# Performance work log

Measured on AMD Instinct MI355X. Metric: run time of the kernel, lower is better.

Reference implementation:

```python
import jax, jax.numpy as jnp
import numpy as np

NUM_HEADS = 8
EPS = 1e-5


def conv3x3(x, w):
    # x: (b,c,f,w), w: (out_c,in_c,3,3), padding=1, stride=1, no bias
    return jax.lax.conv_general_dilated(
        x, w, window_strides=(1, 1), padding=((1, 1), (1, 1)),
        dimension_numbers=('NCHW', 'OIHW', 'NCHW'))


def mc_layernorm(x, g, b):
    # MultichannelLayerNorm: layernorm over the feature axis (dim 2),
    # per-(channel, feature) affine.
    m = jnp.mean(x, axis=2, keepdims=True)
    v = jnp.var(x, axis=2, keepdims=True)
    xn = (x - m) * jax.lax.rsqrt(v + EPS)
    return xn * g[None, :, :, None] + b[None, :, :, None]


def mc_linear(x, wp, wd=None):
    # per-channel feature linear: y[b,c,g,w] = sum_f wp[c,g,f] x[b,c,f,w]
    y = jnp.einsum('bcfw,cgf->bcgw', x, wp)
    if wd is not None:  # depthwise=True adds 1x1 cross-channel mix
        y = jnp.einsum('bcfw,oc->bofw', y, wd)
    return y


def _split_heads(t):
    # (b,c,f,w) -> (b,c,w,H,dh); matches transpose(2,3).reshape(b,c,w,H,-1)
    b, c, f, w = t.shape
    return jnp.transpose(t, (0, 1, 3, 2)).reshape(b, c, w, NUM_HEADS, f // NUM_HEADS)


def _forward(x, conv_q, conv_k, conv_v, wq, wk, wv, wo_pw, wo_dw,
             g1, b1, g2, b2, w1_pw, w1_dw, w2_pw):
    b, c, f, w = x.shape
    # --- attention (MultichannelMultiheadAttention, prev_qk=None) ---
    n1 = mc_layernorm(x, g1, b1)
    q = _split_heads(mc_linear(conv3x3(n1, conv_q), wq))  # (b,c,w,H,dh)
    k = _split_heads(mc_linear(conv3x3(n1, conv_k), wk))
    v = _split_heads(mc_linear(conv3x3(n1, conv_v), wv))
    # qk: (b,c,H,w,w); scaled by sqrt(features) (torch uses sqrt(h)=height)
    qk = jnp.einsum('bcqhd,bckhd->bchqk', q, k) / jnp.sqrt(jnp.float32(f))
    a = jnp.einsum('bchqk,bckhd->bcqhd', jax.nn.softmax(qk, axis=-1), v)
    a = jnp.transpose(a.reshape(b, c, w, f), (0, 1, 3, 2))  # (b,c,f,w)
    z = mc_linear(a, wo_pw, wo_dw)  # o_proj, depthwise=True
    h = x + z  # dropout is identity in eval
    # --- FFN with SquaredReLU ---
    n2 = mc_layernorm(h, g2, b2)
    u = mc_linear(n2, w1_pw, w1_dw)          # (b,c,4f,w)
    u = jnp.square(jax.nn.relu(u))           # SquaredReLU
    z = mc_linear(u, w2_pw)                  # (b,c,f,w)
    h = h + z
    return h, qk


def setup_inputs() -> dict:
    key = jax.random.key(0)
    ks = jax.random.split(key, 12)
    b, c, f, w = 2, 16, 256, 512
    e = 4 * f
    s_conv = 1.0 / np.sqrt(c * 9)
    s_f = 1.0 / np.sqrt(f)
    s_e = 1.0 / np.sqrt(e)
    s_c = 1.0 / np.sqrt(c)
    return {
        'x': jax.random.normal(ks[0], (b, c, f, w), jnp.float32),
        'conv_q': jax.random.normal(ks[1], (c, c, 3, 3), jnp.float32) * s_conv,
        'conv_k': jax.random.normal(ks[2], (c, c, 3, 3), jnp.float32) * s_conv,
        'conv_v': jax.random.normal(ks[3], (c, c, 3, 3), jnp.float32) * s_conv,
        'wq': jax.random.normal(ks[4], (c, f, f), jnp.float32) * s_f,
        'wk': jax.random.normal(ks[5], (c, f, f), jnp.float32) * s_f,
        'wv': jax.random.normal(ks[6], (c, f, f), jnp.float32) * s_f,
        'wo_pw': jax.random.normal(ks[7], (c, f, f), jnp.float32) * s_f,
        'wo_dw': jax.random.normal(ks[8], (c, c), jnp.float32) * s_c,
        'g1': jnp.ones((c, f), jnp.float32),
        'b1': jnp.zeros((c, f), jnp.float32),
        'g2': jnp.ones((c, f), jnp.float32),
        'b2': jnp.zeros((c, f), jnp.float32),
        'w1_pw': jax.random.normal(ks[9], (c, e, f), jnp.float32) * s_f,
        'w1_dw': jax.random.normal(ks[10], (c, c), jnp.float32) * s_c,
        'w2_pw': jax.random.normal(ks[11], (c, f, e), jnp.float32) * s_e,
    }


def reference(x, conv_q, conv_k, conv_v, wq, wk, wv, wo_pw, wo_dw,
              g1, b1, g2, b2, w1_pw, w1_dw, w2_pw):
    return _forward(x, conv_q, conv_k, conv_v, wq, wk, wv, wo_pw, wo_dw,
                    g1, b1, g2, b2, w1_pw, w1_dw, w2_pw)
```

## Files before the change

kernel.cpp:

```cpp
#include <hip/hip_runtime.h>

#define BB 2
#define CC 16
#define BC 32
#define FF 256
#define WW 512
#define HH 8
#define DH 32

using bf16x8 = __attribute__((ext_vector_type(8))) __bf16;
using f32x4  = __attribute__((ext_vector_type(4))) float;
using us8    = __attribute__((ext_vector_type(8))) unsigned short;
using us4    = __attribute__((ext_vector_type(4))) unsigned short;

#define AS1 __attribute__((address_space(1)))
#define AS3 __attribute__((address_space(3)))

__device__ __forceinline__ float bf2f(unsigned short u) {
    union { unsigned int i; float f; } x; x.i = ((unsigned int)u) << 16; return x.f;
}
__device__ __forceinline__ unsigned short f2bf(float f) {
    union { float f; unsigned int i; } x; x.f = f;
    unsigned int r = x.i + 0x7fffu + ((x.i >> 16) & 1u);
    return (unsigned short)(r >> 16);
}
__device__ __forceinline__ f32x4 mfma16(bf16x8 a, bf16x8 b, f32x4 c) {
    return __builtin_amdgcn_mfma_f32_16x16x32_bf16(a, b, c, 0, 0, 0);
}
__device__ __forceinline__ void gload16(const void* g, void* l) {
    __builtin_amdgcn_global_load_lds((AS1 void*)g, (AS3 void*)l, 16, 0, 0);
}

__global__ __launch_bounds__(256) void prep_ln(
    const float* __restrict__ x, const float* __restrict__ g1,
    const float* __restrict__ b1, unsigned short* __restrict__ n1,
    const float* __restrict__ wq, const float* __restrict__ wk,
    const float* __restrict__ wv, const float* __restrict__ wo,
    const float* __restrict__ w1, const float* __restrict__ w2,
    const float* __restrict__ cwq, const float* __restrict__ cwk,
    const float* __restrict__ cwv,
    unsigned short* __restrict__ Wqkv, unsigned short* __restrict__ Wo16,
    unsigned short* __restrict__ W116, unsigned short* __restrict__ W216,
    unsigned short* __restrict__ Aw) {
    __shared__ float red[2][4][64];
    __shared__ float mr[2][64];
    int bid = blockIdx.x;
    if (bid < 256) {
        int bc = bid & 31, c = bc & 15;
        int part = threadIdx.x >> 6, wl = threadIdx.x & 63;
        int w = (bid >> 5) * 64 + wl;
        const float* xp = x + ((size_t)bc * FF + part * 64) * WW + w;
        float s = 0.f, s2 = 0.f;
#pragma unroll 4
        for (int i = 0; i < 64; ++i) { float t = xp[(size_t)i * WW]; s += t; s2 += t * t; }
        red[0][part][wl] = s; red[1][part][wl] = s2;
        __syncthreads();
        if (part == 0) {
            float S  = red[0][0][wl] + red[0][1][wl] + red[0][2][wl] + red[0][3][wl];
            float S2 = red[1][0][wl] + red[1][1][wl] + red[1][2][wl] + red[1][3][wl];
            float m = S * (1.f / FF);
            float v = S2 * (1.f / FF) - m * m;
            mr[0][wl] = m; mr[1][wl] = rsqrtf(v + 1e-5f);
        }
        __syncthreads();
        float m = mr[0][wl], r = mr[1][wl];
        const float* gp = g1 + c * FF + part * 64;
        const float* bp = b1 + c * FF + part * 64;
        unsigned short* op = n1 + ((size_t)bc * FF + part * 64) * WW + w;
#pragma unroll 4
        for (int i = 0; i < 64; ++i)
            op[(size_t)i * WW] = f2bf((xp[(size_t)i * WW] - m) * r * gp[i] + bp[i]);
    } else if (bid < 256 + 6144) {
        int i = (bid - 256) * 256 + threadIdx.x;
        const float* s; unsigned short* d; int off;
        if (i < 131072)       { s = wq; d = Wqkv;            off = i; }
        else if (i < 262144)  { s = wk; d = Wqkv + 1048576;  off = i - 131072; }
        else if (i < 393216)  { s = wv; d = Wqkv + 2097152;  off = i - 262144; }
        else if (i < 524288)  { s = wo; d = Wo16;            off = i - 393216; }
        else if (i < 1048576) { s = w1; d = W116;            off = i - 524288; }
        else                  { s = w2; d = W216;            off = i - 1048576; }
        const float4* sp = (const float4*)s + (size_t)off * 2;
        float4 a = sp[0], b = sp[1];
        us8 p;
        p[0] = f2bf(a.x); p[1] = f2bf(a.y); p[2] = f2bf(a.z); p[3] = f2bf(a.w);
        p[4] = f2bf(b.x); p[5] = f2bf(b.y); p[6] = f2bf(b.z); p[7] = f2bf(b.w);
        *((us8*)d + off) = p;
    } else {
        int idx = (bid - 256 - 6144) * 256 + threadIdx.x;
        if (idx < 7680) {
            int tensor = idx / 2560;
            int r = idx - tensor * 2560;
            int tp = r >> 9, co = (r >> 5) & 15, k = r & 31;
            int tap = tp * 2 + (k >> 4), ci = k & 15;
            float v = 0.f;
            if (tap < 9) {
                const float* w = tensor == 0 ? cwq : (tensor == 1 ? cwk : cwv);
                v = w[(co * 16 + ci) * 9 + tap];
            }
            Aw[idx] = f2bf(v);
        }
    }
}

__global__ __launch_bounds__(256) void ln2t_kernel(
    const float* __restrict__ x, const float* __restrict__ g,
    const float* __restrict__ bta, unsigned short* __restrict__ out) {
    __shared__ float red[2][4][64];
    __shared__ float mr[2][64];
    int bc = blockIdx.x, c = bc & 15;
    int part = threadIdx.x >> 6, wl = threadIdx.x & 63;
    int w = blockIdx.y * 64 + wl;
    const float* xp = x + ((size_t)bc * FF + part * 64) * WW + w;
    float s = 0.f, s2 = 0.f;
#pragma unroll 4
    for (int i = 0; i < 64; ++i) { float t = xp[(size_t)i * WW]; s += t; s2 += t * t; }
    red[0][part][wl] = s; red[1][part][wl] = s2;
    __syncthreads();
    if (part == 0) {
        float S  = red[0][0][wl] + red[0][1][wl] + red[0][2][wl] + red[0][3][wl];
        float S2 = red[1][0][wl] + red[1][1][wl] + red[1][2][wl] + red[1][3][wl];
        float m = S * (1.f / FF);
        float v = S2 * (1.f / FF) - m * m;
        mr[0][wl] = m; mr[1][wl] = rsqrtf(v + 1e-5f);
    }
    __syncthreads();
    float m = mr[0][wl], r = mr[1][wl];
    const float* gp = g + c * FF + part * 64;
    const float* bp = bta + c * FF + part * 64;
    unsigned short* op = out + ((size_t)bc * WW + w) * FF + part * 64;
    for (int i8 = 0; i8 < 8; ++i8) {
        us8 pk;
#pragma unroll
        for (int e = 0; e < 8; ++e) {
            int i = i8 * 8 + e;
            pk[e] = f2bf((xp[(size_t)i * WW] - m) * r * gp[i] + bp[i]);
        }
        *(us8*)(op + i8 * 8) = pk;
    }
}

__global__ __launch_bounds__(256) void conv3_mfma(
    const unsigned short* __restrict__ n1, const unsigned short* __restrict__ Aw,
    unsigned short* __restrict__ oq, unsigned short* __restrict__ ok,
    unsigned short* __restrict__ ov) {
    __shared__ __align__(16) unsigned short Xl[6][68][16];
    const int b = blockIdx.z;
    const int f0 = blockIdx.y * 4;
    const int w0 = blockIdx.x * 64;
    const int tx = threadIdx.x;
    const int lane = tx & 63, wid = tx >> 6;
    const int lr = lane & 15, lg = lane >> 4;
    {
        uint4 z{0, 0, 0, 0};
        for (int i = tx; i < 816; i += 256) ((uint4*)Xl)[i] = z;
    }
    __syncthreads();
    if (tx < 240) {
        int c = tx % 10;
        int fr = (tx / 10) % 6;
        int ci0 = (tx / 60) * 4;
        int fy = f0 - 1 + fr;
        int wx = w0 - 8 + c * 8;
        if (fy >= 0 && fy < FF && wx >= 0 && wx <= WW - 8) {
            const unsigned short* base = n1 + ((size_t)(b * CC + ci0) * FF + fy) * WW + wx;
            us8 v0 = *(const us8*)(base);
            us8 v1 = *(const us8*)(base + (size_t)FF * WW);
            us8 v2 = *(const us8*)(base + (size_t)2 * FF * WW);
            us8 v3 = *(const us8*)(base + (size_t)3 * FF * WW);
            if (c >= 1 && c <= 8) {
#pragma unroll
                for (int e = 0; e < 8; ++e) {
                    int wl = c * 8 + e - 7;
                    us4 p; p.x = v0[e]; p.y = v1[e]; p.z = v2[e]; p.w = v3[e];
                    *(us4*)(&Xl[fr][wl][ci0]) = p;
                }
            } else {
#pragma unroll
                for (int e = 0; e < 8; ++e) {
                    int wl = c * 8 + e - 7;
                    if (wl >= 0 && wl < 66) {
                        us4 p; p.x = v0[e]; p.y = v1[e]; p.z = v2[e]; p.w = v3[e];
                        *(us4*)(&Xl[fr][wl][ci0]) = p;
                    }
                }
            }
        }
    }
    __syncthreads();
    bf16x8 A[3][5];
#pragma unroll
    for (int t3 = 0; t3 < 3; ++t3)
#pragma unroll
        for (int t = 0; t < 5; ++t)
            A[t3][t] = *(const bf16x8*)(Aw + ((t3 * 5 + t) * 16 + lr) * 32 + lg * 8);
    const bool h = (lane & 32) != 0;
    int doff[5];
    doff[0] = (h ? (-68 * 32) : ((-68 - 1) * 32));
    doff[1] = (h ? (-1 * 32) : ((-68 + 1) * 32));
    doff[2] = (h ? (1 * 32) : 0);
    doff[3] = (h ? (68 * 32) : ((68 - 1) * 32));
    doff[4] = ((68 + 1) * 32);
    const int fl = wid + 1;
    const int fglob = f0 + wid;
    char* xbase = (char*)Xl + (fl * 68 + 1) * 32 + ((lg & 1) ? 16 : 0);
#pragma unroll
    for (int pt = 0; pt < 4; ++pt) {
        char* bb = xbase + (pt * 16 + lr) * 32;
        bf16x8 Bf[5];
#pragma unroll
        for (int t = 0; t < 5; ++t) Bf[t] = *(const bf16x8*)(bb + doff[t]);
        f32x4 aq = {0.f, 0.f, 0.f, 0.f}, ak = {0.f, 0.f, 0.f, 0.f}, av = {0.f, 0.f, 0.f, 0.f};
#pragma unroll
        for (int t = 0; t < 5; ++t) {
            aq = mfma16(A[0][t], Bf[t], aq);
            ak = mfma16(A[1][t], Bf[t], ak);
            av = mfma16(A[2][t], Bf[t], av);
        }
        int w = w0 + pt * 16 + lr;
#pragma unroll
        for (int r = 0; r < 4; ++r) {
            int co = lg * 4 + r;
            size_t o = ((size_t)(b * CC + co) * FF + fglob) * WW + w;
            oq[o] = f2bf(aq[r]);
            ok[o] = f2bf(ak[r]);
            ov[o] = f2bf(av[r]);
        }
    }
}

template <int K, int BSRC, int MODE, int NT>
__global__ __launch_bounds__(256, 4) void mgemm3(
    const unsigned short* __restrict__ Wb, const unsigned short* __restrict__ T,
    unsigned short* __restrict__ ob, float* __restrict__ of) {
    constexpr int M = 256;
    __shared__ __align__(16) unsigned short Al[64 * 64];
    __shared__ __align__(16) unsigned short Bl[128 * 64];
    const int id = blockIdx.x;
    const int grp = ((id >> 5) << 3) | (id & 7);
    const int g = (id >> 3) & 3;
    const int t = (NT > 1) ? (grp >> 7) : 0;
    const int rem = grp & 127;
    const int bc = rem >> 2, z = rem & 3;
    const int c = bc & 15;
    const int G0 = g * 64, W0 = z * 128;
    const int tx = threadIdx.x;
    const int lane = tx & 63, wid = tx >> 6;
    const int lr = lane & 15, lg = lane >> 4;
    const int wr = wid >> 1, wc = wid & 1;
    const unsigned short* Ab = Wb + (size_t)t * 1048576 + ((size_t)c * M + G0) * K;
    const unsigned short* Tt = T + (size_t)t * 4194304;
    f32x4 acc[2][4];
#pragma unroll
    for (int i = 0; i < 2; ++i)
#pragma unroll
        for (int j = 0; j < 4; ++j) acc[i][j] = (f32x4){0.f, 0.f, 0.f, 0.f};

    const int arow0 = tx >> 3;

    for (int f0 = 0; f0 < K; f0 += 64) {
#pragma unroll
        for (int rep = 0; rep < 2; ++rep) {
            int row = arow0 + rep * 32;
            int seg = (tx & 7) ^ (row & 7);
            gload16(Ab + (size_t)row * K + f0 + seg * 8,
                    (char*)Al + wid * 1024 + rep * 4096);
        }
        if (BSRC == 0) {
            const unsigned short* Tb = Tt + ((size_t)bc * WW + W0) * K;
#pragma unroll
            for (int rep = 0; rep < 4; ++rep) {
                int row = arow0 + rep * 32;
                int seg = (tx & 7) ^ (row & 7) ^ ((row >> 3) & 7);
                gload16(Tb + (size_t)row * K + f0 + seg * 8,
                        (char*)Bl + wid * 1024 + rep * 4096);
            }
        } else {
            const unsigned short* Tb = Tt + (size_t)bc * K * WW;
            const int wseg = tx & 15, fgrp = tx >> 4;
            us8 tv[4];
#pragma unroll
            for (int i = 0; i < 4; ++i)
                tv[i] = *(const us8*)(Tb + (size_t)(f0 + fgrp * 4 + i) * WW + W0 + wseg * 8);
#pragma unroll
            for (int j = 0; j < 8; ++j) {
                int w = wseg * 8 + j;
                us4 p; p.x = tv[0][j]; p.y = tv[1][j]; p.z = tv[2][j]; p.w = tv[3][j];
                *(us4*)((char*)Bl + w * 128 +
                        ((((fgrp >> 1) ^ (w & 7) ^ ((w >> 3) & 7)) << 4)) + (fgrp & 1) * 8) = p;
            }
        }
        __syncthreads();
#pragma unroll
        for (int kc = 0; kc < 2; ++kc) {
            bf16x8 af[2], bf[4];
#pragma unroll
            for (int i = 0; i < 2; ++i) {
                int gr = wr * 32 + i * 16 + lr;
                af[i] = *(const bf16x8*)((char*)Al + gr * 128 +
                        (((kc * 4 + lg) ^ (gr & 7)) << 4));
            }
#pragma unroll
            for (int j = 0; j < 4; ++j) {
                int wrw = wc * 64 + j * 16 + lr;
                bf[j] = *(const bf16x8*)((char*)Bl + wrw * 128 +
                        (((kc * 4 + lg) ^ (wrw & 7) ^ ((wrw >> 3) & 7)) << 4));
            }
#pragma unroll
            for (int i = 0; i < 2; ++i)
#pragma unroll
                for (int j = 0; j < 4; ++j)
                    acc[i][j] = mfma16(af[i], bf[j], acc[i][j]);
        }
        __syncthreads();
    }
#pragma unroll
    for (int i = 0; i < 2; ++i)
#pragma unroll
        for (int j = 0; j < 4; ++j) {
            int g2 = G0 + wr * 32 + i * 16 + lg * 4;
            int w = W0 + wc * 64 + j * 16 + lr;
#pragma unroll
            for (int r = 0; r < 4; ++r) {
                size_t o = (size_t)t * 4194304 + ((size_t)bc * M + g2 + r) * WW + w;
                if (MODE == 0) ob[o] = f2bf(acc[i][j][r]);
                else of[o] += acc[i][j][r];
            }
        }
}

template <int K, int M, int MODE>
__global__ __launch_bounds__(256, 2) void mgemm2(
    const unsigned short* __restrict__ Wb, const unsigned short* __restrict__ T,
    unsigned short* __restrict__ ob, float* __restrict__ of) {
    __shared__ __align__(16) unsigned short SH[2][128 * 64];
    unsigned short* Al = SH[0];
    unsigned short* Bl = SH[1];
    const int id = blockIdx.x;
    const int grp = ((id >> 6) << 3) | (id & 7);
    const int g = (id >> 3) & 7;
    const int bc = grp >> 2, z = grp & 3;
    const int c = bc & 15;
    const int G0 = g * 128, W0 = z * 128;
    const int tx = threadIdx.x;
    const int lane = tx & 63, wid = tx >> 6;
    const int lr = lane & 15, lg = lane >> 4;
    const int wr = wid >> 1, wc = wid & 1;
    const unsigned short* Ab = Wb + ((size_t)c * M + G0) * K;
    f32x4 acc[4][4];
#pragma unroll
    for (int i = 0; i < 4; ++i)
#pragma unroll
        for (int j = 0; j < 4; ++j) acc[i][j] = (f32x4){0.f, 0.f, 0.f, 0.f};

    const int arow0 = tx >> 3;

    for (int f0 = 0; f0 < K; f0 += 64) {
#pragma unroll
        for (int rep = 0; rep < 4; ++rep) {
            int row = arow0 + rep * 32;
            int seg = (tx & 7) ^ (row & 7);
            gload16(Ab + (size_t)row * K + f0 + seg * 8,
                    (char*)Al + wid * 1024 + rep * 4096);
        }
        {
            const unsigned short* Tb = T + ((size_t)bc * WW + W0) * K;
#pragma unroll
            for (int rep = 0; rep < 4; ++rep) {
                int row = arow0 + rep * 32;
                int seg = (tx & 7) ^ (row & 7) ^ ((row >> 3) & 7);
                gload16(Tb + (size_t)row * K + f0 + seg * 8,
                        (char*)Bl + wid * 1024 + rep * 4096);
            }
        }
        __syncthreads();
#pragma unroll
        for (int kc = 0; kc < 2; ++kc) {
            bf16x8 af[4], bf[4];
#pragma unroll
            for (int i = 0; i < 4; ++i) {
                int gr = wr * 64 + i * 16 + lr;
                af[i] = *(const bf16x8*)((char*)Al + gr * 128 +
                        (((kc * 4 + lg) ^ (gr & 7)) << 4));
                int wrw = wc * 64 + i * 16 + lr;
                bf[i] = *(const bf16x8*)((char*)Bl + wrw * 128 +
                        (((kc * 4 + lg) ^ (wrw & 7) ^ ((wrw >> 3) & 7)) << 4));
            }
#pragma unroll
            for (int i = 0; i < 4; ++i)
#pragma unroll
                for (int j = 0; j < 4; ++j)
                    acc[i][j] = mfma16(af[i], bf[j], acc[i][j]);
        }
        __syncthreads();
    }
    if (MODE == 2) {
        char* S = (char*)SH;
#pragma unroll
        for (int i = 0; i < 4; ++i)
#pragma unroll
            for (int j = 0; j < 4; ++j) {
                int wl = wc * 64 + j * 16 + lr;
                int gl = wr * 64 + i * 16 + lg * 4;
                us4 pk;
                pk.x = f2bf(acc[i][j][0]); pk.y = f2bf(acc[i][j][1]);
                pk.z = f2bf(acc[i][j][2]); pk.w = f2bf(acc[i][j][3]);
                *(us4*)(S + wl * 256 + ((gl * 2) ^ ((wl & 7) << 4))) = pk;
            }
        __syncthreads();
        unsigned short* og = ob + ((size_t)bc * WW + W0) * M + G0;
#pragma unroll
        for (int rep = 0; rep < 8; ++rep) {
            int slot = tx + rep * 256;
            int row = slot >> 4, col = slot & 15;
            us8 v = *(const us8*)(S + row * 256 + ((col * 16) ^ ((row & 7) << 4)));
            *(us8*)(og + (size_t)row * M + col * 8) = v;
        }
    } else {
#pragma unroll
        for (int i = 0; i < 4; ++i)
#pragma unroll
            for (int j = 0; j < 4; ++j) {
                int gg = G0 + wr * 64 + i * 16 + lg * 4;
                int w = W0 + wc * 64 + j * 16 + lr;
#pragma unroll
                for (int r = 0; r < 4; ++r) {
                    size_t o = ((size_t)bc * M + gg + r) * WW + w;
                    if (MODE == 0) ob[o] = f2bf(acc[i][j][r]);
                    else of[o] += acc[i][j][r];
                }
            }
    }
}

__global__ __launch_bounds__(256, 2) void attn_fused(
    const unsigned short* __restrict__ qb, const unsigned short* __restrict__ kb,
    const unsigned short* __restrict__ vb, float* __restrict__ qko,
    unsigned short* __restrict__ abT) {
    __shared__ unsigned short Kl[512 * 32];
    __shared__ unsigned short Vl[32 * 512];
    __shared__ unsigned short Ql[64 * 32];
    const int bch = blockIdx.x, qt = blockIdx.y;
    const int bc = bch >> 3, h = bch & 7;
    const int tx = threadIdx.x;
    const int lane = tx & 63, wid = tx >> 6;
    const int lr = lane & 15, lg = lane >> 4;

    const unsigned short* kbase = kb + ((size_t)bc * FF + h * DH) * WW;
    const unsigned short* vbase = vb + ((size_t)bc * FF + h * DH) * WW;
    const unsigned short* qbase = qb + ((size_t)bc * FF + h * DH) * WW + qt * 64;

    {
        int d0 = ((tx >> 3) & 7) * 4;
#pragma unroll
        for (int rep = 0; rep < 2; ++rep) {
            int kw0 = (tx & 7) * 8 + ((tx >> 6) & 3) * 64 + rep * 256;
            us8 v0 = *(const us8*)(kbase + (size_t)(d0 + 0) * WW + kw0);
            us8 v1 = *(const us8*)(kbase + (size_t)(d0 + 1) * WW + kw0);
            us8 v2 = *(const us8*)(kbase + (size_t)(d0 + 2) * WW + kw0);
            us8 v3 = *(const us8*)(kbase + (size_t)(d0 + 3) * WW + kw0);
#pragma unroll
            for (int j = 0; j < 8; ++j) {
                int kw = kw0 + j;
                us4 p; p.x = v0[j]; p.y = v1[j]; p.z = v2[j]; p.w = v3[j];
                *(us4*)((char*)Kl + kw * 64 + ((d0 * 2) ^ ((kw & 3) << 4))) = p;
            }
        }
    }
    {
        int d = tx >> 3;
        int sw = (d & 7) << 4;
#pragma unroll
        for (int rep = 0; rep < 8; ++rep) {
            int kw0 = (tx & 7) * 8 + rep * 64;
            us8 tv = *(const us8*)(vbase + (size_t)d * WW + kw0);
            *(us8*)((char*)Vl + d * 1024 + ((kw0 * 2) ^ sw)) = tv;
        }
    }
    if (tx < 64) {
        int d0 = ((tx >> 3) & 7) * 4;
        int q0 = (tx & 7) * 8;
        us8 v0 = *(const us8*)(qbase + (size_t)(d0 + 0) * WW + q0);
        us8 v1 = *(const us8*)(qbase + (size_t)(d0 + 1) * WW + q0);
        us8 v2 = *(const us8*)(qbase + (size_t)(d0 + 2) * WW + q0);
        us8 v3 = *(const us8*)(qbase + (size_t)(d0 + 3) * WW + q0);
#pragma unroll
        for (int j = 0; j < 8; ++j) {
            us4 p; p.x = v0[j]; p.y = v1[j]; p.z = v2[j]; p.w = v3[j];
            *(us4*)(&Ql[(q0 + j) * 32 + d0]) = p;
        }
    }
    __syncthreads();

    const int q0w = wid * 16;
    bf16x8 qf = *(const bf16x8*)((char*)Ql + (q0w + lr) * 64 + lg * 16);
    f32x4 s[32];
#pragma unroll
    for (int i = 0; i < 32; ++i) s[i] = (f32x4){0.f, 0.f, 0.f, 0.f};
#pragma unroll
    for (int kwt = 0; kwt < 32; ++kwt) {
        int krow = kwt * 16 + lr;
        bf16x8 kf = *(const bf16x8*)((char*)Kl + krow * 64 + ((lg * 16) ^ ((krow & 3) << 4)));
        s[kwt] = mfma16(kf, qf, s[kwt]);
    }
    float mx = -3.0e38f;
    float* qrow = qko + ((size_t)bch * WW + qt * 64 + q0w + lr) * WW;
#pragma unroll
    for (int kwt = 0; kwt < 32; ++kwt) {
        s[kwt] *= 0.0625f;
        float4 st;
        st.x = s[kwt][0]; st.y = s[kwt][1]; st.z = s[kwt][2]; st.w = s[kwt][3];
        *(float4*)(qrow + kwt * 16 + lg * 4) = st;
        mx = fmaxf(mx, fmaxf(fmaxf(st.x, st.y), fmaxf(st.z, st.w)));
    }
    mx = fmaxf(mx, __shfl_xor(mx, 16));
    mx = fmaxf(mx, __shfl_xor(mx, 32));
    float sum = 0.f;
#pragma unroll
    for (int kwt = 0; kwt < 32; ++kwt) {
#pragma unroll
        for (int r = 0; r < 4; ++r) {
            float p = __expf(s[kwt][r] - mx);
            s[kwt][r] = p;
            sum += p;
        }
    }
    sum += __shfl_xor(sum, 16);
    sum += __shfl_xor(sum, 32);
    float inv = 1.0f / sum;

    f32x4 av[2];
    av[0] = (f32x4){0.f, 0.f, 0.f, 0.f};
    av[1] = (f32x4){0.f, 0.f, 0.f, 0.f};
#pragma unroll
    for (int t = 0; t < 16; ++t) {
        unsigned pa0 = f2bf(s[2 * t][0]) | ((unsigned)f2bf(s[2 * t][1]) << 16);
        unsigned pa1 = f2bf(s[2 * t][2]) | ((unsigned)f2bf(s[2 * t][3]) << 16);
        unsigned pb0 = f2bf(s[2 * t + 1][0]) | ((unsigned)f2bf(s[2 * t + 1][1]) << 16);
        unsigned pb1 = f2bf(s[2 * t + 1][2]) | ((unsigned)f2bf(s[2 * t + 1][3]) << 16);
        unsigned s16_0 = (lg == 1) ? pa0 : pb0, s16_1 = (lg == 1) ? pa1 : pb1;
        unsigned s32_0 = (lg == 3) ? pa0 : pb0, s32_1 = (lg == 3) ? pa1 : pb1;
        unsigned s48_0 = (lg == 2) ? pa0 : pb0, s48_1 = (lg == 2) ? pa1 : pb1;
        unsigned r16_0 = (unsigned)__shfl_xor((int)s16_0, 16);
        unsigned r16_1 = (unsigned)__shfl_xor((int)s16_1, 16);
        unsigned r32_0 = (unsigned)__shfl_xor((int)s32_0, 32);
        unsigned r32_1 = (unsigned)__shfl_xor((int)s32_1, 32);
        unsigned r48_0 = (unsigned)__shfl_xor((int)s48_0, 48);
        unsigned r48_1 = (unsigned)__shfl_xor((int)s48_1, 48);
        uint4 wv;
        if (lg == 0)      { wv.x = pa0;   wv.y = pa1;   wv.z = r16_0; wv.w = r16_1; }
        else if (lg == 1) { wv.x = r48_0; wv.y = r48_1; wv.z = r32_0; wv.w = r32_1; }
        else if (lg == 2) { wv.x = r32_0; wv.y = r32_1; wv.z = r48_0; wv.w = r48_1; }
        else              { wv.x = r16_0; wv.y = r16_1; wv.z = pb0;  wv.w = pb1; }
        bf16x8 pf = *reinterpret_cast<bf16x8*>(&wv);
#pragma unroll
        for (int di = 0; di < 2; ++di) {
            int vr = di * 16 + lr;
            bf16x8 vf = *(const bf16x8*)((char*)Vl + vr * 1024 + ((t * 64 + lg * 16) ^ ((vr & 7) << 4)));
            av[di] = mfma16(vf, pf, av[di]);
        }
    }
    unsigned short* arow = abT + ((size_t)bc * WW + qt * 64 + q0w + lr) * FF + h * DH;
#pragma unroll
    for (int di = 0; di < 2; ++di) {
        us4 pk;
        pk.x = f2bf(av[di][0] * inv); pk.y = f2bf(av[di][1] * inv);
        pk.z = f2bf(av[di][2] * inv); pk.w = f2bf(av[di][3] * inv);
        *(us4*)(arow + di * 16 + lg * 4) = pk;
    }
}

template <int NPC, int MODE>
__global__ __launch_bounds__(256) void dwmix(
    const unsigned short* __restrict__ in, const float* __restrict__ wdw,
    const float* __restrict__ x, float* __restrict__ fo, unsigned short* __restrict__ bo) {
    __shared__ unsigned short L[16][1024];
    int b = blockIdx.y;
    size_t base = (size_t)blockIdx.x * 1024;
    int tx = threadIdx.x;
#pragma unroll
    for (int r = 0; r < 8; ++r) {
        int idx = tx + r * 256;
        int ci = idx >> 7;
        int seg = idx & 127;
        *(us8*)&L[ci][seg * 8] = *(const us8*)(in + ((size_t)(b * 16 + ci)) * NPC + base + seg * 8);
    }
    __syncthreads();
#pragma unroll
    for (int pos = 0; pos < 4; ++pos) {
        int fw = tx + pos * 256;
        float vin[16];
#pragma unroll
        for (int ci = 0; ci < 16; ++ci) vin[ci] = bf2f(L[ci][fw]);
#pragma unroll
        for (int o = 0; o < 16; ++o) {
            float s = 0.f;
#pragma unroll
            for (int ci = 0; ci < 16; ++ci) s += wdw[o * 16 + ci] * vin[ci];
            size_t oi = ((size_t)(b * 16 + o)) * NPC + base + fw;
            if (MODE == 0) fo[oi] = x[oi] + s;
            else { s = fmaxf(s, 0.f); bo[oi] = f2bf(s * s); }
        }
    }
}

extern "C" void kernel_launch(void* const* d_in, const int* in_sizes, int n_in,
                              void* d_out, int out_size, void* d_ws, size_t ws_size,
                              hipStream_t stream) {
    const float* x      = (const float*)d_in[0];
    const float* conv_q = (const float*)d_in[1];
    const float* conv_k = (const float*)d_in[2];
    const float* conv_v = (const float*)d_in[3];
    const float* wq     = (const float*)d_in[4];
    const float* wk     = (const float*)d_in[5];
    const float* wv     = (const float*)d_in[6];
    const float* wo_pw  = (const float*)d_in[7];
    const float* wo_dw  = (const float*)d_in[8];
    const float* g1     = (const float*)d_in[9];
    const float* b1     = (const float*)d_in[10];
    const float* g2     = (const float*)d_in[11];
    const float* b2     = (const float*)d_in[12];
    const float* w1_pw  = (const float*)d_in[13];
    const float* w1_dw  = (const float*)d_in[14];
    const float* w2_pw  = (const float*)d_in[15];

    float* hout  = (float*)d_out;
    float* qkout = (float*)d_out + 4194304;

    char* ws = (char*)d_ws;
    const size_t MB1 = (size_t)1 << 20;
    unsigned short* n1   = (unsigned short*)(ws + 0 * MB1);
    unsigned short* cq   = (unsigned short*)(ws + 8 * MB1);
    unsigned short* qb   = (unsigned short*)(ws + 32 * MB1);
    unsigned short* kb   = (unsigned short*)(ws + 40 * MB1);
    unsigned short* vb   = (unsigned short*)(ws + 48 * MB1);
    unsigned short* abT  = (unsigned short*)(ws + 56 * MB1);
    unsigned short* pwb  = (unsigned short*)(ws + 64 * MB1);
    unsigned short* n2t  = (unsigned short*)(ws + 72 * MB1);
    unsigned short* u1t  = (unsigned short*)(ws + 80 * MB1);
    unsigned short* u2t  = (unsigned short*)(ws + 112 * MB1);
    unsigned short* Wqkv = (unsigned short*)(ws + 144 * MB1);
    unsigned short* Wo16 = (unsigned short*)(ws + 150 * MB1);
    unsigned short* W116 = (unsigned short*)(ws + 152 * MB1);
    unsigned short* W216 = (unsigned short*)(ws + 160 * MB1);
    unsigned short* Awb  = (unsigned short*)(ws + 168 * MB1);

    prep_ln<<<dim3(6430), 256, 0, stream>>>(x, g1, b1, n1,
                                            wq, wk, wv, wo_pw, w1_pw, w2_pw,
                                            conv_q, conv_k, conv_v,
                                            Wqkv, Wo16, W116, W216, Awb);
    conv3_mfma<<<dim3(8, 64, BB), 256, 0, stream>>>(n1, Awb, cq, cq + 4194304, cq + 8388608);
    mgemm3<256, 1, 0, 3><<<dim3(1536), 256, 0, stream>>>(Wqkv, cq, qb, nullptr);
    attn_fused<<<dim3(BC * HH, 8), 256, 0, stream>>>(qb, kb, vb, qkout, abT);
    mgemm3<256, 0, 0, 1><<<dim3(512), 256, 0, stream>>>(Wo16, abT, pwb, nullptr);
    dwmix<131072, 0><<<dim3(128, BB), 256, 0, stream>>>(pwb, wo_dw, x, hout, nullptr);
    ln2t_kernel<<<dim3(BC, 8), 256, 0, stream>>>(hout, g2, b2, n2t);
    mgemm2<256, 1024, 2><<<dim3(1024), 256, 0, stream>>>(W116, n2t, u1t, nullptr);
    dwmix<524288, 1><<<dim3(512, BB), 256, 0, stream>>>(u1t, w1_dw, nullptr, nullptr, u2t);
    mgemm3<1024, 0, 1, 1><<<dim3(512), 256, 0, stream>>>(W216, u2t, nullptr, hout);
}
```

Measured before the change: 269.2 us.

## Double-buffer mgemm3 K-loop, read V from global, and enlarge grids of small kernels

mgemm3 gets double-buffered LDS tiles so the next K-slice loads while the current one runs its MFMAs, and its occupancy hint drops from 4 to 3 blocks to make room for the larger LDS footprint. attn_fused stops staging V in LDS and reads V fragments directly from global memory, which frees LDS. The layernorm kernels now use 32-wide column tiles and dwmix gets a tile template, so the first dwmix launch uses 256-element tiles. Together these give more blocks for the bandwidth-bound kernels. The costs are more LDS per mgemm3 block, lower occupancy, and uncoalesced V reads in attention.

```diff
diff --git a/kernel.cpp b/kernel.cpp
--- a/kernel.cpp
+++ b/kernel.cpp
@@ -42,36 +42,37 @@
     unsigned short* __restrict__ Wqkv, unsigned short* __restrict__ Wo16,
     unsigned short* __restrict__ W116, unsigned short* __restrict__ W216,
     unsigned short* __restrict__ Aw) {
-    __shared__ float red[2][4][64];
-    __shared__ float mr[2][64];
+    __shared__ float red[2][8][32];
+    __shared__ float mr[2][32];
     int bid = blockIdx.x;
-    if (bid < 256) {
+    if (bid < 512) {
         int bc = bid & 31, c = bc & 15;
-        int part = threadIdx.x >> 6, wl = threadIdx.x & 63;
-        int w = (bid >> 5) * 64 + wl;
-        const float* xp = x + ((size_t)bc * FF + part * 64) * WW + w;
+        int part = threadIdx.x >> 5, wl = threadIdx.x & 31;
+        int w = (bid >> 5) * 32 + wl;
+        const float* xp = x + ((size_t)bc * FF + part * 32) * WW + w;
         float s = 0.f, s2 = 0.f;
 #pragma unroll 4
-        for (int i = 0; i < 64; ++i) { float t = xp[(size_t)i * WW]; s += t; s2 += t * t; }
+        for (int i = 0; i < 32; ++i) { float t = xp[(size_t)i * WW]; s += t; s2 += t * t; }
         red[0][part][wl] = s; red[1][part][wl] = s2;
         __syncthreads();
         if (part == 0) {
-            float S  = red[0][0][wl] + red[0][1][wl] + red[0][2][wl] + red[0][3][wl];
-            float S2 = red[1][0][wl] + red[1][1][wl] + red[1][2][wl] + red[1][3][wl];
+            float S = 0.f, S2 = 0.f;
+#pragma unroll
+            for (int p = 0; p < 8; ++p) { S += red[0][p][wl]; S2 += red[1][p][wl]; }
             float m = S * (1.f / FF);
             float v = S2 * (1.f / FF) - m * m;
             mr[0][wl] = m; mr[1][wl] = rsqrtf(v + 1e-5f);
         }
         __syncthreads();
         float m = mr[0][wl], r = mr[1][wl];
-        const float* gp = g1 + c * FF + part * 64;
-        const float* bp = b1 + c * FF + part * 64;
-        unsigned short* op = n1 + ((size_t)bc * FF + part * 64) * WW + w;
+        const float* gp = g1 + c * FF + part * 32;
+        const float* bp = b1 + c * FF + part * 32;
+        unsigned short* op = n1 + ((size_t)bc * FF + part * 32) * WW + w;
 #pragma unroll 4
-        for (int i = 0; i < 64; ++i)
+        for (int i = 0; i < 32; ++i)
             op[(size_t)i * WW] = f2bf((xp[(size_t)i * WW] - m) * r * gp[i] + bp[i]);
-    } else if (bid < 256 + 6144) {
-        int i = (bid - 256) * 256 + threadIdx.x;
+    } else if (bid < 512 + 6144) {
+        int i = (bid - 512) * 256 + threadIdx.x;
         const float* s; unsigned short* d; int off;
         if (i < 131072)       { s = wq; d = Wqkv;            off = i; }
         else if (i < 262144)  { s = wk; d = Wqkv + 1048576;  off = i - 131072; }
@@ -86,7 +87,7 @@
         p[4] = f2bf(b.x); p[5] = f2bf(b.y); p[6] = f2bf(b.z); p[7] = f2bf(b.w);
         *((us8*)d + off) = p;
     } else {
-        int idx = (bid - 256 - 6144) * 256 + threadIdx.x;
+        int idx = (bid - 512 - 6144) * 256 + threadIdx.x;
         if (idx < 7680) {
             int tensor = idx / 2560;
             int r = idx - tensor * 2560;
@@ -105,30 +106,31 @@
 __global__ __launch_bounds__(256) void ln2t_kernel(
     const float* __restrict__ x, const float* __restrict__ g,
     const float* __restrict__ bta, unsigned short* __restrict__ out) {
-    __shared__ float red[2][4][64];
-    __shared__ float mr[2][64];
+    __shared__ float red[2][8][32];
+    __shared__ float mr[2][32];
     int bc = blockIdx.x, c = bc & 15;
-    int part = threadIdx.x >> 6, wl = threadIdx.x & 63;
-    int w = blockIdx.y * 64 + wl;
-    const float* xp = x + ((size_t)bc * FF + part * 64) * WW + w;
+    int part = threadIdx.x >> 5, wl = threadIdx.x & 31;
+    int w = blockIdx.y * 32 + wl;
+    const float* xp = x + ((size_t)bc * FF + part * 32) * WW + w;
     float s = 0.f, s2 = 0.f;
 #pragma unroll 4
-    for (int i = 0; i < 64; ++i) { float t = xp[(size_t)i * WW]; s += t; s2 += t * t; }
+    for (int i = 0; i < 32; ++i) { float t = xp[(size_t)i * WW]; s += t; s2 += t * t; }
     red[0][part][wl] = s; red[1][part][wl] = s2;
     __syncthreads();
     if (part == 0) {
-        float S  = red[0][0][wl] + red[0][1][wl] + red[0][2][wl] + red[0][3][wl];
-        float S2 = red[1][0][wl] + red[1][1][wl] + red[1][2][wl] + red[1][3][wl];
+        float S = 0.f, S2 = 0.f;
+#pragma unroll
+        for (int p = 0; p < 8; ++p) { S += red[0][p][wl]; S2 += red[1][p][wl]; }
         float m = S * (1.f / FF);
         float v = S2 * (1.f / FF) - m * m;
         mr[0][wl] = m; mr[1][wl] = rsqrtf(v + 1e-5f);
     }
     __syncthreads();
     float m = mr[0][wl], r = mr[1][wl];
-    const float* gp = g + c * FF + part * 64;
-    const float* bp = bta + c * FF + part * 64;
-    unsigned short* op = out + ((size_t)bc * WW + w) * FF + part * 64;
-    for (int i8 = 0; i8 < 8; ++i8) {
+    const float* gp = g + c * FF + part * 32;
+    const float* bp = bta + c * FF + part * 32;
+    unsigned short* op = out + ((size_t)bc * WW + w) * FF + part * 32;
+    for (int i8 = 0; i8 < 4; ++i8) {
         us8 pk;
 #pragma unroll
         for (int e = 0; e < 8; ++e) {
@@ -229,12 +231,13 @@
 }
 
 template <int K, int BSRC, int MODE, int NT>
-__global__ __launch_bounds__(256, 4) void mgemm3(
+__global__ __launch_bounds__(256, 3) void mgemm3(
     const unsigned short* __restrict__ Wb, const unsigned short* __restrict__ T,
     unsigned short* __restrict__ ob, float* __restrict__ of) {
     constexpr int M = 256;
-    __shared__ __align__(16) unsigned short Al[64 * 64];
-    __shared__ __align__(16) unsigned short Bl[128 * 64];
+    constexpr int NK = K / 64;
+    __shared__ __align__(16) unsigned short Al[2][64 * 64];
+    __shared__ __align__(16) unsigned short Bl[2][128 * 64];
     const int id = blockIdx.x;
     const int grp = ((id >> 5) << 3) | (id & 7);
     const int g = (id >> 3) & 3;
@@ -249,60 +252,70 @@
     const int wr = wid >> 1, wc = wid & 1;
     const unsigned short* Ab = Wb + (size_t)t * 1048576 + ((size_t)c * M + G0) * K;
     const unsigned short* Tt = T + (size_t)t * 4194304;
+    const unsigned short* TbB0 = Tt + ((size_t)bc * WW + W0) * K;
+    const unsigned short* TbB1 = Tt + (size_t)bc * K * WW;
+    const int arow0 = tx >> 3;
+    const int wseg = tx & 15, fgrp = tx >> 4;
     f32x4 acc[2][4];
 #pragma unroll
     for (int i = 0; i < 2; ++i)
 #pragma unroll
         for (int j = 0; j < 4; ++j) acc[i][j] = (f32x4){0.f, 0.f, 0.f, 0.f};
 
-    const int arow0 = tx >> 3;
-
-    for (int f0 = 0; f0 < K; f0 += 64) {
-#pragma unroll
-        for (int rep = 0; rep < 2; ++rep) {
-            int row = arow0 + rep * 32;
-            int seg = (tx & 7) ^ (row & 7);
-            gload16(Ab + (size_t)row * K + f0 + seg * 8,
-                    (char*)Al + wid * 1024 + rep * 4096);
-        }
-        if (BSRC == 0) {
-            const unsigned short* Tb = Tt + ((size_t)bc * WW + W0) * K;
-#pragma unroll
-            for (int rep = 0; rep < 4; ++rep) {
-                int row = arow0 + rep * 32;
-                int seg = (tx & 7) ^ (row & 7) ^ ((row >> 3) & 7);
-                gload16(Tb + (size_t)row * K + f0 + seg * 8,
-                        (char*)Bl + wid * 1024 + rep * 4096);
-            }
-        } else {
-            const unsigned short* Tb = Tt + (size_t)bc * K * WW;
-            const int wseg = tx & 15, fgrp = tx >> 4;
-            us8 tv[4];
-#pragma unroll
-            for (int i = 0; i < 4; ++i)
-                tv[i] = *(const us8*)(Tb + (size_t)(f0 + fgrp * 4 + i) * WW + W0 + wseg * 8);
-#pragma unroll
-            for (int j = 0; j < 8; ++j) {
-                int w = wseg * 8 + j;
-                us4 p; p.x = tv[0][j]; p.y = tv[1][j]; p.z = tv[2][j]; p.w = tv[3][j];
-                *(us4*)((char*)Bl + w * 128 +
-                        ((((fgrp >> 1) ^ (w & 7) ^ ((w >> 3) & 7)) << 4)) + (fgrp & 1) * 8) = p;
-            }
-        }
-        __syncthreads();
+#define STAGE_A(buf, f0)                                                     \
+    _Pragma("unroll")                                                        \
+    for (int rep = 0; rep < 2; ++rep) {                                      \
+        int row = arow0 + rep * 32;                                          \
+        int seg = (tx & 7) ^ (row & 7);                                      \
+        gload16(Ab + (size_t)row * K + (f0) + seg * 8,                       \
+                (char*)Al[buf] + wid * 1024 + rep * 4096);                   \
+    }
+#define STAGE_B0(buf, f0)                                                    \
+    _Pragma("unroll")                                                        \
+    for (int rep = 0; rep < 4; ++rep) {                                      \
+        int row = arow0 + rep * 32;                                          \
+        int seg = (tx & 7) ^ (row & 7) ^ ((row >> 3) & 7);                   \
+        gload16(TbB0 + (size_t)row * K + (f0) + seg * 8,                     \
+                (char*)Bl[buf] + wid * 1024 + rep * 4096);                   \
+    }
+#define GATHER_B1(f0)                                                        \
+    _Pragma("unroll")                                                        \
+    for (int i = 0; i < 4; ++i)                                              \
+        tv[i] = *(const us8*)(TbB1 + (size_t)((f0) + fgrp * 4 + i) * WW + W0 + wseg * 8);
+#define WRITE_B1(buf)                                                        \
+    _Pragma("unroll")                                                        \
+    for (int j = 0; j < 8; ++j) {                                            \
+        int w = wseg * 8 + j;                                                \
+        us4 p; p.x = tv[0][j]; p.y = tv[1][j]; p.z = tv[2][j]; p.w = tv[3][j]; \
+        *(us4*)((char*)Bl[buf] + w * 128 +                                   \
+                ((((fgrp >> 1) ^ (w & 7) ^ ((w >> 3) & 7)) << 4)) + (fgrp & 1) * 8) = p; \
+    }
+
+    us8 tv[4];
+    STAGE_A(0, 0)
+    if (BSRC == 0) { STAGE_B0(0, 0) } else { GATHER_B1(0) WRITE_B1(0) }
+    __syncthreads();
+    int cur = 0;
+    for (int k = 0; k < NK; ++k) {
+        const int f0n = (k + 1) * 64;
+        if (k + 1 < NK) {
+            STAGE_A(cur ^ 1, f0n)
+            if (BSRC == 0) { STAGE_B0(cur ^ 1, f0n) }
+            else { GATHER_B1(f0n) }
+        }
 #pragma unroll
         for (int kc = 0; kc < 2; ++kc) {
             bf16x8 af[2], bf[4];
 #pragma unroll
             for (int i = 0; i < 2; ++i) {
                 int gr = wr * 32 + i * 16 + lr;
-                af[i] = *(const bf16x8*)((char*)Al + gr * 128 +
+                af[i] = *(const bf16x8*)((char*)Al[cur] + gr * 128 +
                         (((kc * 4 + lg) ^ (gr & 7)) << 4));
             }
 #pragma unroll
             for (int j = 0; j < 4; ++j) {
                 int wrw = wc * 64 + j * 16 + lr;
-                bf[j] = *(const bf16x8*)((char*)Bl + wrw * 128 +
+                bf[j] = *(const bf16x8*)((char*)Bl[cur] + wrw * 128 +
                         (((kc * 4 + lg) ^ (wrw & 7) ^ ((wrw >> 3) & 7)) << 4));
             }
 #pragma unroll
@@ -311,8 +324,14 @@
                 for (int j = 0; j < 4; ++j)
                     acc[i][j] = mfma16(af[i], bf[j], acc[i][j]);
         }
+        if (BSRC == 1 && k + 1 < NK) { WRITE_B1(cur ^ 1) }
         __syncthreads();
-    }
+        cur ^= 1;
+    }
+#undef STAGE_A
+#undef STAGE_B0
+#undef GATHER_B1
+#undef WRITE_B1
 #pragma unroll
     for (int i = 0; i < 2; ++i)
 #pragma unroll
@@ -437,7 +456,6 @@
     const unsigned short* __restrict__ vb, float* __restrict__ qko,
     unsigned short* __restrict__ abT) {
     __shared__ unsigned short Kl[512 * 32];
-    __shared__ unsigned short Vl[32 * 512];
     __shared__ unsigned short Ql[64 * 32];
     const int bch = blockIdx.x, qt = blockIdx.y;
     const int bc = bch >> 3, h = bch & 7;
@@ -464,16 +482,6 @@
                 us4 p; p.x = v0[j]; p.y = v1[j]; p.z = v2[j]; p.w = v3[j];
                 *(us4*)((char*)Kl + kw * 64 + ((d0 * 2) ^ ((kw & 3) << 4))) = p;
             }
-        }
-    }
-    {
-        int d = tx >> 3;
-        int sw = (d & 7) << 4;
-#pragma unroll
-        for (int rep = 0; rep < 8; ++rep) {
-            int kw0 = (tx & 7) * 8 + rep * 64;
-            us8 tv = *(const us8*)(vbase + (size_t)d * WW + kw0);
-            *(us8*)((char*)Vl + d * 1024 + ((kw0 * 2) ^ sw)) = tv;
         }
     }
     if (tx < 64) {
@@ -555,7 +563,7 @@
 #pragma unroll
         for (int di = 0; di < 2; ++di) {
             int vr = di * 16 + lr;
-            bf16x8 vf = *(const bf16x8*)((char*)Vl + vr * 1024 + ((t * 64 + lg * 16) ^ ((vr & 7) << 4)));
+            bf16x8 vf = *(const bf16x8*)(vbase + (size_t)vr * WW + t * 32 + lg * 8);
             av[di] = mfma16(vf, pf, av[di]);
         }
     }
@@ -569,24 +577,27 @@
     }
 }
 
-template <int NPC, int MODE>
+template <int NPC, int MODE, int TILE>
 __global__ __launch_bounds__(256) void dwmix(
     const unsigned short* __restrict__ in, const float* __restrict__ wdw,
     const float* __restrict__ x, float* __restrict__ fo, unsigned short* __restrict__ bo) {
-    __shared__ unsigned short L[16][1024];
+    __shared__ unsigned short L[16][TILE];
+    constexpr int C8 = TILE / 8;
+    constexpr int LV = TILE / 128;
+    constexpr int PER = TILE / 256;
     int b = blockIdx.y;
-    size_t base = (size_t)blockIdx.x * 1024;
+    size_t base = (size_t)blockIdx.x * TILE;
     int tx = threadIdx.x;
 #pragma unroll
-    for (int r = 0; r < 8; ++r) {
+    for (int r = 0; r < LV; ++r) {
         int idx = tx + r * 256;
-        int ci = idx >> 7;
-        int seg = idx & 127;
+        int ci = idx / C8;
+        int seg = idx % C8;
         *(us8*)&L[ci][seg * 8] = *(const us8*)(in + ((size_t)(b * 16 + ci)) * NPC + base + seg * 8);
     }
     __syncthreads();
 #pragma unroll
-    for (int pos = 0; pos < 4; ++pos) {
+    for (int pos = 0; pos < PER; ++pos) {
         int fw = tx + pos * 256;
         float vin[16];
 #pragma unroll
@@ -644,7 +655,7 @@
     unsigned short* W216 = (unsigned short*)(ws + 160 * MB1);
     unsigned short* Awb  = (unsigned short*)(ws + 168 * MB1);
 
-    prep_ln<<<dim3(6430), 256, 0, stream>>>(x, g1, b1, n1,
+    prep_ln<<<dim3(6686), 256, 0, stream>>>(x, g1, b1, n1,
                                             wq, wk, wv, wo_pw, w1_pw, w2_pw,
                                             conv_q, conv_k, conv_v,
                                             Wqkv, Wo16, W116, W216, Awb);
@@ -652,9 +663,9 @@
     mgemm3<256, 1, 0, 3><<<dim3(1536), 256, 0, stream>>>(Wqkv, cq, qb, nullptr);
     attn_fused<<<dim3(BC * HH, 8), 256, 0, stream>>>(qb, kb, vb, qkout, abT);
     mgemm3<256, 0, 0, 1><<<dim3(512), 256, 0, stream>>>(Wo16, abT, pwb, nullptr);
-    dwmix<131072, 0><<<dim3(128, BB), 256, 0, stream>>>(pwb, wo_dw, x, hout, nullptr);
-    ln2t_kernel<<<dim3(BC, 8), 256, 0, stream>>>(hout, g2, b2, n2t);
+    dwmix<131072, 0, 256><<<dim3(512, BB), 256, 0, stream>>>(pwb, wo_dw, x, hout, nullptr);
+    ln2t_kernel<<<dim3(BC, 16), 256, 0, stream>>>(hout, g2, b2, n2t);
     mgemm2<256, 1024, 2><<<dim3(1024), 256, 0, stream>>>(W116, n2t, u1t, nullptr);
-    dwmix<524288, 1><<<dim3(512, BB), 256, 0, stream>>>(u1t, w1_dw, nullptr, nullptr, u2t);
+    dwmix<524288, 1, 1024><<<dim3(512, BB), 256, 0, stream>>>(u1t, w1_dw, nullptr, nullptr, u2t);
     mgemm3<1024, 0, 1, 1><<<dim3(512), 256, 0, stream>>>(W216, u2t, nullptr, hout);
 }
```

Measured after the change: 261.8 us (median of 2 runs). -2.7%, faster.
